# Performance work log

Measured on AMD Instinct MI355X. Metric: run time of the kernel, lower is better.

## Reference

```python
import jax, jax.numpy as jnp
import numpy as np
import math

# config constants (from init_kwargs)
W_ROSE, W_QUALITY, W_VOLUME = 0.5, 0.3, 0.2
EPS = 1e-8
DEGEN_EPS = 1e-8


def _rose_score(v):
    # v: [N, n, d] -> [N]; centroid-based radial cosine rose score
    n = v.shape[-2]
    centroid = v.mean(axis=-2, keepdims=True)
    radial = v - centroid
    norms = jnp.clip(jnp.linalg.norm(radial, axis=-1, keepdims=True), EPS)
    u = radial / norms
    cos = jnp.einsum('...id,...jd->...ij', u, u)            # [N, n, n]
    diag = jnp.einsum('...ii->...', cos)
    cos_mean = (cos.sum(axis=(-1, -2)) - diag) / (n * (n - 1))  # off-diagonal mean
    return (cos_mean + 1.0) * 0.5


def _pairwise_sq_dists(v):
    diff = v[..., :, None, :] - v[..., None, :, :]
    return jnp.sum(diff * diff, axis=-1)                    # [N, n, n]


def _regularity(v):
    # SimplexQuality regularity: min_edge / max_edge (1.0 for a regular simplex)
    n = v.shape[-2]
    d = jnp.sqrt(jnp.clip(_pairwise_sq_dists(v), 1e-12))
    off = ~np.eye(n, dtype=bool)                            # static boolean mask
    edges = d[..., off]                                     # [N, n*(n-1)]
    return edges.min(axis=-1) / jnp.clip(edges.max(axis=-1), EPS)


def _cayley_menger_volume(v):
    # v: [N, n, d]; k-simplex with k = n-1; Cayley-Menger determinant volume
    n = v.shape[-2]
    k = n - 1
    d2 = _pairwise_sq_dists(v)                              # [N, n, n]
    bs = d2.shape[:-2]
    top = jnp.concatenate([jnp.zeros(bs + (1, 1), d2.dtype),
                           jnp.ones(bs + (1, n), d2.dtype)], axis=-1)
    bot = jnp.concatenate([jnp.ones(bs + (n, 1), d2.dtype), d2], axis=-1)
    cm = jnp.concatenate([top, bot], axis=-2)               # [N, n+1, n+1]
    det = jnp.linalg.det(cm)
    coeff = ((-1.0) ** (k + 1)) / (2.0 ** k * float(math.factorial(k)) ** 2)
    v2 = coeff * det
    vol = jnp.sqrt(jnp.clip(v2, 0.0))
    is_degenerate = vol < DEGEN_EPS
    return vol, is_degenerate


def setup_inputs() -> dict:
    key = jax.random.key(0)
    k1, k2 = jax.random.split(key)
    B, O, K1, D = 16, 8192, 5, 64
    n_samples = int(O * 0.25)  # 2048
    predicted_simplices = jax.random.normal(k1, (B, O, K1, D), dtype=jnp.float32)
    sample_indices = jax.random.randint(k2, (B, n_samples), 0, O, dtype=jnp.int32)
    return {"predicted_simplices": predicted_simplices,
            "sample_indices": sample_indices}


def reference(predicted_simplices, sample_indices):
    B, O, K1, D = predicted_simplices.shape
    n_samples = sample_indices.shape[1]
    # per-batch gather of sampled simplices (replaces torch per-batch loop)
    sampled = predicted_simplices[jnp.arange(B)[:, None], sample_indices]  # [B, S, K1, D]
    flat = sampled.reshape(B * n_samples, K1, D)

    rose = _rose_score(flat)
    rose_loss = (1.0 - rose).mean()

    regularity = _regularity(flat)
    quality_loss = (1.0 - regularity).mean()

    vol, is_degenerate = _cayley_menger_volume(flat)
    volume_loss = is_degenerate.astype(flat.dtype).mean()

    total_loss = W_ROSE * rose_loss + W_QUALITY * quality_loss + W_VOLUME * volume_loss
    return total_loss
```

## Files before the change

kernel.cpp:

```cpp
#include <hip/hip_runtime.h>

#define K1 5
#define DIM 64
#define OCNT 8192
#define NS 2048
#define BLOCK 256

__device__ __forceinline__ double det4(const double m[4][4]) {
    double c01 = m[2][0] * m[3][1] - m[2][1] * m[3][0];
    double c02 = m[2][0] * m[3][2] - m[2][2] * m[3][0];
    double c03 = m[2][0] * m[3][3] - m[2][3] * m[3][0];
    double c12 = m[2][1] * m[3][2] - m[2][2] * m[3][1];
    double c13 = m[2][1] * m[3][3] - m[2][3] * m[3][1];
    double c23 = m[2][2] * m[3][3] - m[2][3] * m[3][2];
    double d0 = m[1][1] * c23 - m[1][2] * c13 + m[1][3] * c12;
    double d1 = m[1][0] * c23 - m[1][2] * c03 + m[1][3] * c02;
    double d2 = m[1][0] * c13 - m[1][1] * c03 + m[1][3] * c01;
    double d3 = m[1][0] * c12 - m[1][1] * c02 + m[1][2] * c01;
    return m[0][0] * d0 - m[0][1] * d1 + m[0][2] * d2 - m[0][3] * d3;
}

__global__ __launch_bounds__(BLOCK) void cm_main_kernel(
        const float* __restrict__ pts,
        const int* __restrict__ sidx,
        float* __restrict__ block_sums) {
    const int t = blockIdx.x * BLOCK + threadIdx.x;
    const int b = t >> 11;
    const int o = sidx[t];
    const float* base = pts + ((size_t)b * OCNT + (size_t)o) * (K1 * DIM);

    float acc[15];
#pragma unroll
    for (int i = 0; i < 15; ++i) acc[i] = 0.0f;

#pragma unroll
    for (int d0 = 0; d0 < DIM; d0 += 4) {
        float4 x[K1];
#pragma unroll
        for (int i = 0; i < K1; ++i)
            x[i] = *reinterpret_cast<const float4*>(base + i * DIM + d0);
        const float* xf = reinterpret_cast<const float*>(x);
#pragma unroll
        for (int c = 0; c < 4; ++c) {
            float y0 = xf[0 * 4 + c], y1 = xf[1 * 4 + c], y2 = xf[2 * 4 + c],
                  y3 = xf[3 * 4 + c], y4 = xf[4 * 4 + c];
            acc[0]  = fmaf(y0, y0, acc[0]);
            acc[1]  = fmaf(y0, y1, acc[1]);
            acc[2]  = fmaf(y0, y2, acc[2]);
            acc[3]  = fmaf(y0, y3, acc[3]);
            acc[4]  = fmaf(y0, y4, acc[4]);
            acc[5]  = fmaf(y1, y1, acc[5]);
            acc[6]  = fmaf(y1, y2, acc[6]);
            acc[7]  = fmaf(y1, y3, acc[7]);
            acc[8]  = fmaf(y1, y4, acc[8]);
            acc[9]  = fmaf(y2, y2, acc[9]);
            acc[10] = fmaf(y2, y3, acc[10]);
            acc[11] = fmaf(y2, y4, acc[11]);
            acc[12] = fmaf(y3, y3, acc[12]);
            acc[13] = fmaf(y3, y4, acc[13]);
            acc[14] = fmaf(y4, y4, acc[14]);
        }
    }

    float G[K1][K1];
    {
        int k = 0;
#pragma unroll
        for (int i = 0; i < K1; ++i)
#pragma unroll
            for (int j = i; j < K1; ++j) {
                G[i][j] = acc[k];
                G[j][i] = acc[k];
                ++k;
            }
    }

    float S[K1];
    float T = 0.0f;
#pragma unroll
    for (int i = 0; i < K1; ++i) {
        S[i] = G[i][0] + G[i][1] + G[i][2] + G[i][3] + G[i][4];
        T += S[i];
    }
    float ci[K1];
#pragma unroll
    for (int i = 0; i < K1; ++i) ci[i] = S[i] * 0.2f;
    const float cc = T * 0.04f;

    float nrm[K1];
#pragma unroll
    for (int i = 0; i < K1; ++i) {
        float r2 = G[i][i] - 2.0f * ci[i] + cc;
        r2 = fmaxf(r2, 0.0f);
        nrm[i] = fmaxf(sqrtf(r2), 1e-8f);
    }
    float sumcos = 0.0f;
#pragma unroll
    for (int i = 0; i < K1; ++i)
#pragma unroll
        for (int j = i + 1; j < K1; ++j) {
            float num = G[i][j] - ci[i] - ci[j] + cc;
            sumcos += num / (nrm[i] * nrm[j]);
        }
    const float rose = (sumcos * 0.1f + 1.0f) * 0.5f;

    float dmin = 3.4e38f, dmax = 0.0f;
#pragma unroll
    for (int i = 0; i < K1; ++i)
#pragma unroll
        for (int j = i + 1; j < K1; ++j) {
            float d2 = G[i][i] + G[j][j] - 2.0f * G[i][j];
            float dd = sqrtf(fmaxf(d2, 1e-12f));
            dmin = fminf(dmin, dd);
            dmax = fmaxf(dmax, dd);
        }
    const float reg = dmin / fmaxf(dmax, 1e-8f);

    double W[4][4];
#pragma unroll
    for (int a = 1; a < K1; ++a)
#pragma unroll
        for (int c = 1; c < K1; ++c)
            W[a - 1][c - 1] =
                (double)G[a][c] - (double)G[a][0] - (double)G[0][c] + (double)G[0][0];
    double dW = det4(W);
    double vol = sqrt(fmax(dW, 0.0)) * (1.0 / 24.0);
    const float degen = (vol < 1e-8) ? 1.0f : 0.0f;

    float loss = 0.5f * (1.0f - rose) + 0.3f * (1.0f - reg) + 0.2f * degen;

#pragma unroll
    for (int off = 32; off > 0; off >>= 1)
        loss += __shfl_down(loss, off, 64);
    __shared__ float wsum[BLOCK / 64];
    const int lane = threadIdx.x & 63;
    const int wave = threadIdx.x >> 6;
    if (lane == 0) wsum[wave] = loss;
    __syncthreads();
    if (threadIdx.x == 0) {
        float s = 0.0f;
#pragma unroll
        for (int w = 0; w < BLOCK / 64; ++w) s += wsum[w];
        block_sums[blockIdx.x] = s;
    }
}

__global__ __launch_bounds__(128) void cm_final_kernel(
        const float* __restrict__ block_sums, float* __restrict__ out,
        int nblocks, float inv_n) {
    float v = (threadIdx.x < (unsigned)nblocks) ? block_sums[threadIdx.x] : 0.0f;
#pragma unroll
    for (int off = 32; off > 0; off >>= 1)
        v += __shfl_down(v, off, 64);
    __shared__ float wsum[2];
    const int lane = threadIdx.x & 63;
    const int wave = threadIdx.x >> 6;
    if (lane == 0) wsum[wave] = v;
    __syncthreads();
    if (threadIdx.x == 0) out[0] = (wsum[0] + wsum[1]) * inv_n;
}

extern "C" void kernel_launch(void* const* d_in, const int* in_sizes, int n_in,
                              void* d_out, int out_size, void* d_ws, size_t ws_size,
                              hipStream_t stream) {
    const float* pts = (const float*)d_in[0];
    const int* sidx  = (const int*)d_in[1];
    float* out = (float*)d_out;
    float* block_sums = (float*)d_ws;

    const int nsimp = in_sizes[1];
    const int nblocks = nsimp / BLOCK;

    cm_main_kernel<<<nblocks, BLOCK, 0, stream>>>(pts, sidx, block_sums);
    cm_final_kernel<<<1, 128, 0, stream>>>(block_sums, out, nblocks,
                                           1.0f / (float)nsimp);
}
```

Measured before the change: 221.8 us.

## Split each simplex across 16 lanes with coalesced loads and shuffle reduction

Each simplex's 5x64 point block is now handled by 16 lanes, each loading one float4 per vertex, so a wavefront's loads are contiguous instead of strided by 1280 bytes per thread. Partial Gram entries are combined with xor-shuffles, and only lane 0 of each group contributes to the loss sum. The grid grows 16x (32768 simplices need 2048 blocks instead of 128), which exposes far more parallelism for a memory-bound gather. The final reduction kernel now loops over more block sums. The tail math (including the FP64 determinant) is computed redundantly by all 16 lanes.

```diff
diff --git a/kernel.cpp b/kernel.cpp
--- a/kernel.cpp
+++ b/kernel.cpp
@@ -3,8 +3,9 @@
 #define K1 5
 #define DIM 64
 #define OCNT 8192
-#define NS 2048
+#define NSAMP_PER_B 2048
 #define BLOCK 256
+#define LANES_PER_SIMPLEX 16
 
 __device__ __forceinline__ double det4(const double m[4][4]) {
     double c01 = m[2][0] * m[3][1] - m[2][1] * m[3][0];
@@ -24,42 +25,36 @@
         const float* __restrict__ pts,
         const int* __restrict__ sidx,
         float* __restrict__ block_sums) {
-    const int t = blockIdx.x * BLOCK + threadIdx.x;
+    const int tid = blockIdx.x * BLOCK + threadIdx.x;
+    const int t = tid >> 4;
+    const int g = threadIdx.x & 15;
     const int b = t >> 11;
     const int o = sidx[t];
-    const float* base = pts + ((size_t)b * OCNT + (size_t)o) * (K1 * DIM);
+    const float* base =
+        pts + ((size_t)b * OCNT + (size_t)o) * (K1 * DIM) + g * 4;
+
+    float4 x[K1];
+#pragma unroll
+    for (int i = 0; i < K1; ++i)
+        x[i] = *reinterpret_cast<const float4*>(base + i * DIM);
 
     float acc[15];
-#pragma unroll
-    for (int i = 0; i < 15; ++i) acc[i] = 0.0f;
-
-#pragma unroll
-    for (int d0 = 0; d0 < DIM; d0 += 4) {
-        float4 x[K1];
+    {
+        int k = 0;
 #pragma unroll
         for (int i = 0; i < K1; ++i)
-            x[i] = *reinterpret_cast<const float4*>(base + i * DIM + d0);
-        const float* xf = reinterpret_cast<const float*>(x);
 #pragma unroll
-        for (int c = 0; c < 4; ++c) {
-            float y0 = xf[0 * 4 + c], y1 = xf[1 * 4 + c], y2 = xf[2 * 4 + c],
-                  y3 = xf[3 * 4 + c], y4 = xf[4 * 4 + c];
-            acc[0]  = fmaf(y0, y0, acc[0]);
-            acc[1]  = fmaf(y0, y1, acc[1]);
-            acc[2]  = fmaf(y0, y2, acc[2]);
-            acc[3]  = fmaf(y0, y3, acc[3]);
-            acc[4]  = fmaf(y0, y4, acc[4]);
-            acc[5]  = fmaf(y1, y1, acc[5]);
-            acc[6]  = fmaf(y1, y2, acc[6]);
-            acc[7]  = fmaf(y1, y3, acc[7]);
-            acc[8]  = fmaf(y1, y4, acc[8]);
-            acc[9]  = fmaf(y2, y2, acc[9]);
-            acc[10] = fmaf(y2, y3, acc[10]);
-            acc[11] = fmaf(y2, y4, acc[11]);
-            acc[12] = fmaf(y3, y3, acc[12]);
-            acc[13] = fmaf(y3, y4, acc[13]);
-            acc[14] = fmaf(y4, y4, acc[14]);
-        }
+            for (int j = i; j < K1; ++j) {
+                acc[k] = x[i].x * x[j].x + x[i].y * x[j].y +
+                         x[i].z * x[j].z + x[i].w * x[j].w;
+                ++k;
+            }
+    }
+#pragma unroll
+    for (int mask = 1; mask < LANES_PER_SIMPLEX; mask <<= 1) {
+#pragma unroll
+        for (int k = 0; k < 15; ++k)
+            acc[k] += __shfl_xor(acc[k], mask, 64);
     }
 
     float G[K1][K1];
@@ -129,9 +124,11 @@
 
     float loss = 0.5f * (1.0f - rose) + 0.3f * (1.0f - reg) + 0.2f * degen;
 
+    loss = (g == 0) ? loss : 0.0f;
 #pragma unroll
     for (int off = 32; off > 0; off >>= 1)
         loss += __shfl_down(loss, off, 64);
+
     __shared__ float wsum[BLOCK / 64];
     const int lane = threadIdx.x & 63;
     const int wave = threadIdx.x >> 6;
@@ -145,19 +142,25 @@
     }
 }
 
-__global__ __launch_bounds__(128) void cm_final_kernel(
+__global__ __launch_bounds__(BLOCK) void cm_final_kernel(
         const float* __restrict__ block_sums, float* __restrict__ out,
         int nblocks, float inv_n) {
-    float v = (threadIdx.x < (unsigned)nblocks) ? block_sums[threadIdx.x] : 0.0f;
+    float v = 0.0f;
+    for (int i = threadIdx.x; i < nblocks; i += BLOCK) v += block_sums[i];
 #pragma unroll
     for (int off = 32; off > 0; off >>= 1)
         v += __shfl_down(v, off, 64);
-    __shared__ float wsum[2];
+    __shared__ float wsum[BLOCK / 64];
     const int lane = threadIdx.x & 63;
     const int wave = threadIdx.x >> 6;
     if (lane == 0) wsum[wave] = v;
     __syncthreads();
-    if (threadIdx.x == 0) out[0] = (wsum[0] + wsum[1]) * inv_n;
+    if (threadIdx.x == 0) {
+        float s = 0.0f;
+#pragma unroll
+        for (int w = 0; w < BLOCK / 64; ++w) s += wsum[w];
+        out[0] = s * inv_n;
+    }
 }
 
 extern "C" void kernel_launch(void* const* d_in, const int* in_sizes, int n_in,
@@ -169,9 +172,9 @@
     float* block_sums = (float*)d_ws;
 
     const int nsimp = in_sizes[1];
-    const int nblocks = nsimp / BLOCK;
+    const int nblocks = nsimp * LANES_PER_SIMPLEX / BLOCK;
 
     cm_main_kernel<<<nblocks, BLOCK, 0, stream>>>(pts, sidx, block_sums);
-    cm_final_kernel<<<1, 128, 0, stream>>>(block_sums, out, nblocks,
-                                           1.0f / (float)nsimp);
+    cm_final_kernel<<<1, BLOCK, 0, stream>>>(block_sums, out, nblocks,
+                                             1.0f / (float)nsimp);
 }
```

Result: faster. 209.3 us (-5.6%).
